# Kernel tuning notes

Measured on AMD Instinct MI355X. Metric: run time of the kernel, lower is better.

Reference implementation:

```python
import jax, jax.numpy as jnp
import numpy as np

H = 2048          # hidden_size
I = 1408          # moe_intermediate_size
E = 32            # n_routed_experts
K = 4             # num_experts_per_tok
NS = 2            # n_shared_experts
RG = RU = RD = 128  # CUR ranks
SI = I * NS       # shared-expert intermediate size
B, S = 2, 2048


def _init(key, shape, fan_in):
    return jax.random.normal(key, shape, jnp.float32) / np.sqrt(fan_in)


def setup_inputs() -> dict:
    ks = jax.random.split(jax.random.key(0), 20)
    return {
        'x': jax.random.normal(ks[0], (B, S, H), jnp.float32),
        'gate_w': _init(ks[1], (E, H), H),
        'Rg': _init(ks[2], (RG, H), H),
        'Ru': _init(ks[3], (RU, H), H),
        'Rd': _init(ks[4], (RD, I), I),
        'Ug': _init(ks[5], (E, RG, RG), RG),
        'Cg': _init(ks[6], (E, I, RG), RG),
        'Uu': _init(ks[7], (E, RU, RU), RU),
        'Cu': _init(ks[8], (E, I, RU), RU),
        'Ud': _init(ks[9], (E, RD, RD), RD),
        'Cd': _init(ks[10], (E, H, RD), RD),
        's_Rg': _init(ks[11], (RG, H), H),
        's_Ug': _init(ks[12], (RG, RG), RG),
        's_Cg': _init(ks[13], (SI, RG), RG),
        's_Ru': _init(ks[14], (RU, H), H),
        's_Uu': _init(ks[15], (RU, RU), RU),
        's_Cu': _init(ks[16], (SI, RU), RU),
        's_Rd': _init(ks[17], (RD, SI), SI),
        's_Ud': _init(ks[18], (RD, RD), RD),
        's_Cd': _init(ks[19], (H, RD), RD),
    }


def _moe_forward(x, gate_w, Rg, Ru, Rd, Ug, Cg, Uu, Cu, Ud, Cd,
                 s_Rg, s_Ug, s_Cg, s_Ru, s_Uu, s_Cu, s_Rd, s_Ud, s_Cd):
    Bv, Sv, Hv = x.shape
    xf = x.reshape(-1, Hv)                       # [T,H]
    T = xf.shape[0]

    # ---- top-k softmax gate ----
    logits = xf @ gate_w.T                       # [T,E]
    scores = jax.nn.softmax(logits, axis=-1)
    tw, ti = jax.lax.top_k(scores, K)            # [T,K]
    tw = tw / (tw.sum(-1, keepdims=True) + 1e-20)
    # dense per-(token,expert) combine weight; zero where token not routed.
    # Mathematically identical to the torch gather/per-expert-GEMM/scatter_add path.
    we = jnp.zeros((T, E), xf.dtype).at[jnp.arange(T)[:, None], ti].add(tw)  # [T,E]

    # shared R projections are expert-independent: compute once for all tokens
    rg = xf @ Rg.T                               # [T,RG]
    ru = xf @ Ru.T                               # [T,RU]

    def expert_fn(Ug_e, Cg_e, Uu_e, Cu_e, Ud_e, Cd_e, w_e, rg, ru):
        g = jax.nn.silu((rg @ Ug_e.T) @ Cg_e.T)  # [T,I]
        u = (ru @ Uu_e.T) @ Cu_e.T               # [T,I]
        rd = (g * u) @ Rd.T                      # [T,RD]
        return w_e[:, None] * ((rd @ Ud_e.T) @ Cd_e.T)  # [T,H]

    expert_fn = jax.checkpoint(expert_fn)

    def body(acc, ws):
        Ug_e, Cg_e, Uu_e, Cu_e, Ud_e, Cd_e, w_e = ws
        return acc + expert_fn(Ug_e, Cg_e, Uu_e, Cu_e, Ud_e, Cd_e, w_e, rg, ru), None

    y, _ = jax.lax.scan(body, jnp.zeros_like(xf), (Ug, Cg, Uu, Cu, Ud, Cd, we.T))

    # ---- shared experts (own R matrices, intermediate = I * n_shared) ----
    g = jax.nn.silu(((xf @ s_Rg.T) @ s_Ug.T) @ s_Cg.T)   # [T,SI]
    u = ((xf @ s_Ru.T) @ s_Uu.T) @ s_Cu.T                # [T,SI]
    sh = (((g * u) @ s_Rd.T) @ s_Ud.T) @ s_Cd.T          # [T,H]

    return (y + sh).reshape(Bv, Sv, Hv)


def reference(x, gate_w, Rg, Ru, Rd, Ug, Cg, Uu, Cu, Ud, Cd,
              s_Rg, s_Ug, s_Cg, s_Ru, s_Uu, s_Cu, s_Rd, s_Ud, s_Cd):
    return _moe_forward(x, gate_w, Rg, Ru, Rd, Ug, Cg, Uu, Cu, Ud, Cd,
                        s_Rg, s_Ug, s_Cg, s_Ru, s_Uu, s_Cu, s_Rd, s_Ud, s_Cd)
```

## Files before the change

kernel.cpp:

```cpp
#include <hip/hip_runtime.h>
#include <math.h>

#define T_TOK 4096
#define HD    2048
#define NEXP  32
#define IR    1408
#define ISH   2816
#define NPAIR (T_TOK*4)
#define SRK   136
#define MTILES 11

typedef unsigned short ushort_t;
typedef __attribute__((ext_vector_type(8))) short    short8;
typedef __attribute__((ext_vector_type(8))) __bf16   bf16x8;
typedef __attribute__((ext_vector_type(4))) float    f32x4;

__device__ __forceinline__ f32x4 MF(short8 a, short8 b, f32x4 c) {
  return __builtin_amdgcn_mfma_f32_16x16x32_bf16(
      __builtin_bit_cast(bf16x8, a), __builtin_bit_cast(bf16x8, b), c, 0, 0, 0);
}
__device__ __forceinline__ ushort_t f2b(float f) {
  unsigned u = __float_as_uint(f);
  unsigned r = (u + 0x7fffu + ((u >> 16) & 1u)) >> 16;
  return (ushort_t)r;
}
__device__ __forceinline__ float b2f(ushort_t b) {
  return __uint_as_float(((unsigned)b) << 16);
}

__device__ __forceinline__ void gll16(const ushort_t* g, ushort_t* l) {
  __builtin_amdgcn_global_load_lds(
      (const __attribute__((address_space(1))) unsigned int*)(const void*)g,
      (__attribute__((address_space(3))) unsigned int*)(void*)l, 16, 0, 0);
}

__device__ __forceinline__ void load_64x128_swz(
    const ushort_t* __restrict__ g, size_t gstride, ushort_t* lds, int tid)
{
  const int lane = tid & 63, w = tid >> 6;
  #pragma unroll
  for (int s = 0; s < 4; ++s) {
    int rbase = s*16 + w*4;
    int r = rbase + (lane >> 4);
    int p = lane & 15;
    gll16(g + (size_t)r*gstride + ((p ^ (r & 15)) << 3), lds + rbase*128);
  }
}

__device__ __forceinline__ void load_128x64_swz(
    const ushort_t* __restrict__ g, size_t gstride, ushort_t* lds, int tid)
{
  const int lane = tid & 63, w = tid >> 6;
  #pragma unroll
  for (int s = 0; s < 4; ++s) {
    int rbase = s*32 + w*8;
    int r = rbase + (lane >> 3);
    int p = lane & 7;
    gll16(g + (size_t)r*gstride + ((p ^ (r & 7)) << 3), lds + rbase*64);
  }
}

#define NSEG 19
struct CvtSegs {
  const float* s[NSEG];
  ushort_t* d[NSEG];
  int n4[NSEG];
  int blk0[NSEG+1];
};
__global__ __launch_bounds__(256) void cvt_all_kernel(CvtSegs cs)
{
  int b = blockIdx.x;
  int k = 0;
  #pragma unroll 1
  while (k+1 < NSEG && b >= cs.blk0[k+1]) ++k;
  int i = (b - cs.blk0[k])*256 + threadIdx.x;
  if (i < cs.n4[k]) {
    float4 v = ((const float4*)cs.s[k])[i];
    ushort4 o; o.x=f2b(v.x); o.y=f2b(v.y); o.z=f2b(v.z); o.w=f2b(v.w);
    ((ushort4*)cs.d[k])[i] = o;
  }
}

__global__ __launch_bounds__(256) void gate_kernel(
    const float* __restrict__ x, const float* __restrict__ gw,
    int* __restrict__ topk_idx, float* __restrict__ topk_w, int* __restrict__ cnt)
{
  __shared__ float gws[32*132];
  __shared__ float xs[4*132];
  const int tid = threadIdx.x;
  const int w = tid >> 6, lane = tid & 63;
  const int t0 = blockIdx.x * 4;
  const int e = lane & 31, half = lane >> 5;

  float acc = 0.f;
  for (int ck = 0; ck < HD/128; ++ck) {
    for (int li = tid; li < 1024; li += 256) {
      int r = li >> 5, c4 = li & 31;
      *(float4*)(gws + r*132 + c4*4) = *(const float4*)(gw + (size_t)r*HD + ck*128 + c4*4);
    }
    for (int li = tid; li < 128; li += 256) {
      int r = li >> 5, c4 = li & 31;
      *(float4*)(xs + r*132 + c4*4) = *(const float4*)(x + (size_t)(t0+r)*HD + ck*128 + c4*4);
    }
    __syncthreads();
    #pragma unroll
    for (int k4 = 0; k4 < 16; ++k4) {
      float4 xv = *(const float4*)(xs + w*132 + half*64 + k4*4);
      float4 wv = *(const float4*)(gws + e*132 + half*64 + k4*4);
      acc += xv.x*wv.x + xv.y*wv.y + xv.z*wv.z + xv.w*wv.w;
    }
    __syncthreads();
  }
  float p = acc;
  p += __shfl_down(p, 32);
  float logit = (lane < 32) ? p : -INFINITY;
  float m = logit;
  #pragma unroll
  for (int o = 32; o >= 1; o >>= 1) m = fmaxf(m, __shfl_xor(m, o));
  float ex = (lane < 32) ? expf(logit - m) : 0.f;
  float se = ex;
  #pragma unroll
  for (int o = 32; o >= 1; o >>= 1) se += __shfl_xor(se, o);
  float score = ex / se;

  bool taken = false;
  float selw[4]; int seli[4];
  for (int k = 0; k < 4; ++k) {
    float cur = (lane < 32 && !taken) ? score : -1.f;
    float mm = cur;
    #pragma unroll
    for (int o = 32; o >= 1; o >>= 1) mm = fmaxf(mm, __shfl_xor(mm, o));
    unsigned long long b = __ballot(cur == mm);
    int il = __ffsll(b) - 1;
    if (lane == il) taken = true;
    selw[k] = mm; seli[k] = il;
  }
  float wsum = selw[0]+selw[1]+selw[2]+selw[3] + 1e-20f;
  int t = t0 + w;
  if (lane < 4) {
    topk_idx[t*4+lane] = seli[lane];
    topk_w[t*4+lane]  = selw[lane] / wsum;
    atomicAdd(&cnt[seli[lane]], 1);
  }
}

__global__ void scan_kernel(const int* __restrict__ cnt, int* __restrict__ offA)
{
  if (threadIdx.x == 0) {
    int a = 0;
    for (int e = 0; e < NEXP; ++e) { offA[e] = a; a += cnt[e]; }
    offA[NEXP] = a;
  }
}

__global__ __launch_bounds__(256) void scatter_kernel(
    const int* __restrict__ topk_idx, const float* __restrict__ topk_w,
    const int* __restrict__ offA, int* __restrict__ fill,
    int* __restrict__ list_tok, int* __restrict__ slot_of)
{
  int t = blockIdx.x*256 + threadIdx.x;
  if (t >= T_TOK) return;
  #pragma unroll
  for (int k = 0; k < 4; ++k) {
    int e = topk_idx[t*4+k];
    int pos = atomicAdd(&fill[e], 1);
    int s = offA[e] + pos;
    list_tok[s] = t;
    slot_of[t*4+k] = s;
  }
}

__global__ __launch_bounds__(256) void rproj_kernel(
    const ushort_t* __restrict__ xb,
    const ushort_t* __restrict__ Rg, const ushort_t* __restrict__ Ru,
    const ushort_t* __restrict__ sRg, const ushort_t* __restrict__ sRu,
    ushort_t* __restrict__ rg, ushort_t* __restrict__ ru,
    ushort_t* __restrict__ sa, ushort_t* __restrict__ su)
{
  __shared__ ushort_t abuf[2][64*128];
  const ushort_t* W; ushort_t* Y;
  switch (blockIdx.y) {
    case 0:  W = Rg;  Y = rg; break;
    case 1:  W = Ru;  Y = ru; break;
    case 2:  W = sRg; Y = sa; break;
    default: W = sRu; Y = su; break;
  }
  const int tid = threadIdx.x;
  const int lane = tid & 63, ln = lane & 15, q = lane >> 4;
  const int wv = tid >> 6, mh = wv >> 1, nh = wv & 1;
  const int r0 = blockIdx.x * 64;

  f32x4 acc[2][4];
  #pragma unroll
  for (int i = 0; i < 2; ++i)
    #pragma unroll
    for (int j = 0; j < 4; ++j) acc[i][j] = (f32x4){0.f,0.f,0.f,0.f};

  load_64x128_swz(xb + (size_t)r0*HD, HD, abuf[0], tid);
  for (int kt = 0; kt < 16; ++kt) {
    __syncthreads();
    if (kt+1 < 16)
      load_64x128_swz(xb + (size_t)r0*HD + (kt+1)*128, HD, abuf[(kt+1)&1], tid);
    const ushort_t* A = abuf[kt&1];
    #pragma unroll
    for (int c = 0; c < 4; ++c) {
      short8 a[2], b[4];
      #pragma unroll
      for (int i = 0; i < 2; ++i) {
        int rr = mh*32 + i*16 + ln;
        a[i] = *(const short8*)(A + rr*128 + (((c*4+q) ^ (rr&15)) << 3));
      }
      #pragma unroll
      for (int j = 0; j < 4; ++j)
        b[j] = *(const short8*)(W + (size_t)(nh*64 + j*16 + ln)*HD + kt*128 + c*32 + q*8);
      #pragma unroll
      for (int i = 0; i < 2; ++i)
        #pragma unroll
        for (int j = 0; j < 4; ++j) acc[i][j] = MF(a[i], b[j], acc[i][j]);
    }
  }
  #pragma unroll
  for (int i = 0; i < 2; ++i)
    #pragma unroll
    for (int j = 0; j < 4; ++j)
      #pragma unroll
      for (int r = 0; r < 4; ++r)
        Y[(size_t)(r0 + mh*32 + i*16 + q*4 + r)*128 + nh*64 + j*16 + ln] = f2b(acc[i][j][r]);
}

__device__ __forceinline__ void gemm64x128_regs(
    int tid, const ushort_t* __restrict__ A, const ushort_t* __restrict__ Wg,
    ushort_t* __restrict__ stage, f32x4 acc[2][2][2])
{
  const int lane = tid & 63, ln = lane & 15, q = lane >> 4;
  const int wv = tid >> 6, mh = wv >> 1, nh = wv & 1;
  #pragma unroll
  for (int h = 0; h < 2; ++h)
    #pragma unroll
    for (int i = 0; i < 2; ++i)
      #pragma unroll
      for (int j = 0; j < 2; ++j) acc[h][i][j] = (f32x4){0.f,0.f,0.f,0.f};
  for (int h = 0; h < 2; ++h) {
    for (int li = tid; li < 64*16; li += 256) {
      int r = li >> 4, c = (li & 15) << 3;
      *(short8*)(stage + r*SRK + c) = *(const short8*)(Wg + (size_t)(h*64 + r)*128 + c);
    }
    __syncthreads();
    #pragma unroll
    for (int c = 0; c < 4; ++c) {
      short8 a[2], b[2];
      #pragma unroll
      for (int i = 0; i < 2; ++i)
        a[i] = *(const short8*)(A + (mh*32 + i*16 + ln)*SRK + c*32 + q*8);
      #pragma unroll
      for (int j = 0; j < 2; ++j)
        b[j] = *(const short8*)(stage + (nh*32 + j*16 + ln)*SRK + c*32 + q*8);
      #pragma unroll
      for (int i = 0; i < 2; ++i)
        #pragma unroll
        for (int j = 0; j < 2; ++j) acc[h][i][j] = MF(a[i], b[j], acc[h][i][j]);
    }
    __syncthreads();
  }
}

__global__ __launch_bounds__(256) void pair_proj_kernel(
    const ushort_t* __restrict__ rgb, const ushort_t* __restrict__ rub,
    const ushort_t* __restrict__ sab, const ushort_t* __restrict__ sub,
    const ushort_t* __restrict__ Ug, const ushort_t* __restrict__ Uu,
    const ushort_t* __restrict__ sUg, const ushort_t* __restrict__ sUu,
    const int* __restrict__ offA, const int* __restrict__ cntA,
    const int* __restrict__ list_tok,
    ushort_t* __restrict__ t1R, ushort_t* __restrict__ t2R,
    ushort_t* __restrict__ t1S, ushort_t* __restrict__ t2S)
{
  __shared__ ushort_t ldsX[64*SRK];
  __shared__ ushort_t stage[64*SRK];
  __shared__ int toks[64];
  const int tid = threadIdx.x;
  const int by = blockIdx.y;
  const bool shm = (by == NEXP);
  const int nrows = shm ? T_TOK : cntA[by];
  const int s0 = blockIdx.x * 64;
  if (s0 >= nrows) return;
  const int base = shm ? 0 : offA[by];
  const ushort_t* pUg = shm ? sUg : Ug + (size_t)by*128*128;
  const ushort_t* pUu = shm ? sUu : Uu + (size_t)by*128*128;
  const int lane = tid & 63, ln = lane & 15, q = lane >> 4;
  const int wv = tid >> 6, mh = wv >> 1, nh = wv & 1;

  if (tid < 64) {
    int sc = s0 + tid; if (sc > nrows-1) sc = nrows-1;
    toks[tid] = shm ? sc : list_tok[base + sc];
  }
  __syncthreads();

  f32x4 acc[2][2][2];
  for (int li = tid; li < 64*16; li += 256) {
    int r = li >> 4, c = (li & 15) << 3;
    const ushort_t* src = shm ? sab : rgb;
    *(short8*)(ldsX + r*SRK + c) = *(const short8*)(src + (size_t)toks[r]*128 + c);
  }
  __syncthreads();
  gemm64x128_regs(tid, ldsX, pUg, stage, acc);
  {
    ushort_t* dst = shm ? t1S : (t1R + (size_t)base*128);
    #pragma unroll
    for (int h = 0; h < 2; ++h)
      #pragma unroll
      for (int i = 0; i < 2; ++i)
        #pragma unroll
        for (int r = 0; r < 4; ++r) {
          int gs = s0 + mh*32 + i*16 + q*4 + r;
          if (gs < nrows) {
            #pragma unroll
            for (int j = 0; j < 2; ++j)
              dst[(size_t)gs*128 + h*64 + nh*32 + j*16 + ln] = f2b(acc[h][i][j][r]);
          }
        }
  }
  for (int li = tid; li < 64*16; li += 256) {
    int r = li >> 4, c = (li & 15) << 3;
    const ushort_t* src = shm ? sub : rub;
    *(short8*)(ldsX + r*SRK + c) = *(const short8*)(src + (size_t)toks[r]*128 + c);
  }
  __syncthreads();
  gemm64x128_regs(tid, ldsX, pUu, stage, acc);
  {
    ushort_t* dst = shm ? t2S : (t2R + (size_t)base*128);
    #pragma unroll
    for (int h = 0; h < 2; ++h)
      #pragma unroll
      for (int i = 0; i < 2; ++i)
        #pragma unroll
        for (int r = 0; r < 4; ++r) {
          int gs = s0 + mh*32 + i*16 + q*4 + r;
          if (gs < nrows) {
            #pragma unroll
            for (int j = 0; j < 2; ++j)
              dst[(size_t)gs*128 + h*64 + nh*32 + j*16 + ln] = f2b(acc[h][i][j][r]);
          }
        }
  }
}

__global__ __launch_bounds__(256, 2) void mid_kernel(
    const ushort_t* __restrict__ t1R, const ushort_t* __restrict__ t2R,
    const ushort_t* __restrict__ t1S, const ushort_t* __restrict__ t2S,
    const ushort_t* __restrict__ Cg, const ushort_t* __restrict__ Cu,
    const ushort_t* __restrict__ Rd,
    const ushort_t* __restrict__ sCg, const ushort_t* __restrict__ sCu,
    const ushort_t* __restrict__ sRd,
    const int* __restrict__ offA, const int* __restrict__ cntA,
    float* __restrict__ rdRp, float* __restrict__ rdSp)
{
  __shared__ ushort_t ldsCg[64*128];
  __shared__ ushort_t ldsCu[64*128];
  __shared__ ushort_t ldsRd[128*64];
  __shared__ ushort_t ldsH [64*64];

  const int tid = threadIdx.x;
  const int by = blockIdx.y, bz = blockIdx.z;
  const bool shm = (by == NEXP);
  if (bz >= (shm ? 4 : 2)) return;
  const int nrows = shm ? T_TOK : cntA[by];
  const int s0 = blockIdx.x * 64;
  if (s0 >= nrows) return;
  const int base = shm ? 0 : offA[by];
  const int Ifull = shm ? ISH : IR;
  const ushort_t* pCg = shm ? sCg : Cg + (size_t)by*IR*128;
  const ushort_t* pCu = shm ? sCu : Cu + (size_t)by*IR*128;
  const ushort_t* pRd = shm ? sRd : Rd;

  const int lane = tid & 63, ln = lane & 15, q = lane >> 4;
  const int wv = tid >> 6, mh = wv >> 1, nh = wv & 1;
  const int it0 = bz * MTILES;

  short8 t1f[2][4], t2f[2][4];
  const ushort_t* srcT1 = shm ? t1S : (t1R + (size_t)base*128);
  const ushort_t* srcT2 = shm ? t2S : (t2R + (size_t)base*128);
  #pragma unroll
  for (int i = 0; i < 2; ++i) {
    int r = s0 + mh*32 + i*16 + ln; if (r > nrows-1) r = nrows-1;
    #pragma unroll
    for (int c = 0; c < 4; ++c) {
      t1f[i][c] = *(const short8*)(srcT1 + (size_t)r*128 + c*32 + q*8);
      t2f[i][c] = *(const short8*)(srcT2 + (size_t)r*128 + c*32 + q*8);
    }
  }

  load_64x128_swz(pCg + (size_t)it0*64*128, 128, ldsCg, tid);
  load_64x128_swz(pCu + (size_t)it0*64*128, 128, ldsCu, tid);

  f32x4 rdacc[2][4];
  #pragma unroll
  for (int i = 0; i < 2; ++i)
    #pragma unroll
    for (int j = 0; j < 4; ++j) rdacc[i][j] = (f32x4){0.f,0.f,0.f,0.f};

  __syncthreads();

  for (int it = 0; it < MTILES; ++it) {
    const int i0 = (it0 + it) * 64;
    load_128x64_swz(pRd + i0, Ifull, ldsRd, tid);
    f32x4 g[2][2], u[2][2];
    #pragma unroll
    for (int i = 0; i < 2; ++i)
      #pragma unroll
      for (int j = 0; j < 2; ++j) { g[i][j] = (f32x4){0.f,0.f,0.f,0.f}; u[i][j] = (f32x4){0.f,0.f,0.f,0.f}; }
    #pragma unroll
    for (int c = 0; c < 4; ++c) {
      #pragma unroll
      for (int j = 0; j < 2; ++j) {
        int rr = nh*32 + j*16 + ln;
        int off = rr*128 + (((c*4+q) ^ (rr&15)) << 3);
        short8 bg = *(const short8*)(ldsCg + off);
        short8 bu = *(const short8*)(ldsCu + off);
        #pragma unroll
        for (int i = 0; i < 2; ++i) {
          g[i][j] = MF(t1f[i][c], bg, g[i][j]);
          u[i][j] = MF(t2f[i][c], bu, u[i][j]);
        }
      }
    }
    #pragma unroll
    for (int i = 0; i < 2; ++i)
      #pragma unroll
      for (int j = 0; j < 2; ++j)
        #pragma unroll
        for (int r = 0; r < 4; ++r) {
          float gv = g[i][j][r];
          gv = gv / (1.f + __expf(-gv));
          float hv = gv * u[i][j][r];
          int hr = mh*32 + i*16 + q*4 + r;
          int hc = nh*32 + j*16 + ln;
          ldsH[hr*64 + (((hc>>3) ^ (hr&7)) << 3) + (hc&7)] = f2b(hv);
        }
    __syncthreads();
    if (it+1 < MTILES) {
      load_64x128_swz(pCg + (size_t)(i0+64)*128, 128, ldsCg, tid);
      load_64x128_swz(pCu + (size_t)(i0+64)*128, 128, ldsCu, tid);
    }
    #pragma unroll
    for (int c2 = 0; c2 < 2; ++c2) {
      short8 a[2];
      #pragma unroll
      for (int i = 0; i < 2; ++i) {
        int rr = mh*32 + i*16 + ln;
        a[i] = *(const short8*)(ldsH + rr*64 + (((c2*4+q) ^ (rr&7)) << 3));
      }
      #pragma unroll
      for (int j = 0; j < 4; ++j) {
        int rr = nh*64 + j*16 + ln;
        short8 b = *(const short8*)(ldsRd + rr*64 + (((c2*4+q) ^ (rr&7)) << 3));
        #pragma unroll
        for (int i = 0; i < 2; ++i) rdacc[i][j] = MF(a[i], b, rdacc[i][j]);
      }
    }
    __syncthreads();
  }

  float* dst = shm ? (rdSp + (size_t)bz*T_TOK*128)
                   : (rdRp + (size_t)bz*NPAIR*128 + (size_t)base*128);
  #pragma unroll
  for (int i = 0; i < 2; ++i) {
    #pragma unroll
    for (int r = 0; r < 4; ++r) {
      int gs = s0 + mh*32 + i*16 + q*4 + r;
      if (gs < nrows) {
        #pragma unroll
        for (int j = 0; j < 4; ++j)
          dst[(size_t)gs*128 + nh*64 + j*16 + ln] = rdacc[i][j][r];
      }
    }
  }
}

__global__ __launch_bounds__(256) void out_kernel(
    const float* __restrict__ rdRp, const float* __restrict__ rdSp,
    const ushort_t* __restrict__ Ud, const ushort_t* __restrict__ Cd,
    const ushort_t* __restrict__ sUd, const ushort_t* __restrict__ sCd,
    const int* __restrict__ offA, const int* __restrict__ cntA,
    ushort_t* __restrict__ ybufR, float* __restrict__ out)
{
  __shared__ ushort_t smem[3*64*SRK];
  ushort_t* ldsA  = smem;
  ushort_t* stage = smem + 64*SRK;
  ushort_t* ldsT  = smem + 2*64*SRK;
  ushort_t* cd0   = smem;
  ushort_t* cd1   = smem + 64*128;

  const int tid = threadIdx.x;
  const int by = blockIdx.y;
  const bool shm = (by == NEXP);
  const int nrows = shm ? T_TOK : cntA[by];
  const int s0 = blockIdx.x * 64;
  if (s0 >= nrows) return;
  const int base = shm ? 0 : offA[by];
  const int ct0 = blockIdx.z * 16;
  const ushort_t* pUd = shm ? sUd : Ud + (size_t)by*128*128;
  const ushort_t* pCd = shm ? sCd : Cd + (size_t)by*HD*128;

  const int lane = tid & 63, ln = lane & 15, q = lane >> 4;
  const int wv = tid >> 6, mh = wv >> 1, nh = wv & 1;

  for (int li = tid; li < 64*32; li += 256) {
    int r = li >> 5, c4 = li & 31;
    int row = s0 + r; if (row > nrows-1) row = nrows-1;
    float4 v;
    if (shm) {
      const float* p = rdSp + (size_t)row*128 + c4*4;
      v = *(const float4*)p;
      #pragma unroll
      for (int pp = 1; pp < 4; ++pp) {
        float4 w2 = *(const float4*)(p + (size_t)pp*T_TOK*128);
        v.x += w2.x; v.y += w2.y; v.z += w2.z; v.w += w2.w;
      }
    } else {
      const float* p = rdRp + (size_t)(base+row)*128 + c4*4;
      v = *(const float4*)p;
      float4 w2 = *(const float4*)(p + (size_t)NPAIR*128);
      v.x += w2.x; v.y += w2.y; v.z += w2.z; v.w += w2.w;
    }
    ushort4 o; o.x=f2b(v.x); o.y=f2b(v.y); o.z=f2b(v.z); o.w=f2b(v.w);
    *(ushort4*)(ldsA + r*SRK + c4*4) = o;
  }
  __syncthreads();

  f32x4 acc[2][2][2];
  gemm64x128_regs(tid, ldsA, pUd, stage, acc);
  #pragma unroll
  for (int h = 0; h < 2; ++h)
    #pragma unroll
    for (int i = 0; i < 2; ++i)
      #pragma unroll
      for (int j = 0; j < 2; ++j)
        #pragma unroll
        for (int r = 0; r < 4; ++r)
          ldsT[(mh*32 + i*16 + q*4 + r)*SRK + h*64 + nh*32 + j*16 + ln] = f2b(acc[h][i][j][r]);
  __syncthreads();
  short8 t3f[2][4];
  #pragma unroll
  for (int i = 0; i < 2; ++i)
    #pragma unroll
    for (int c = 0; c < 4; ++c)
      t3f[i][c] = *(const short8*)(ldsT + (mh*32 + i*16 + ln)*SRK + c*32 + q*8);
  __syncthreads();

  load_64x128_swz(pCd + (size_t)ct0*64*128, 128, cd0, tid);
  for (int tt = 0; tt < 16; ++tt) {
    __syncthreads();
    ushort_t* cur = (tt & 1) ? cd1 : cd0;
    ushort_t* nxt = (tt & 1) ? cd0 : cd1;
    if (tt+1 < 16)
      load_64x128_swz(pCd + (size_t)(ct0+tt+1)*64*128, 128, nxt, tid);
    f32x4 y[2][2];
    #pragma unroll
    for (int i = 0; i < 2; ++i)
      #pragma unroll
      for (int j = 0; j < 2; ++j) y[i][j] = (f32x4){0.f,0.f,0.f,0.f};
    #pragma unroll
    for (int c = 0; c < 4; ++c) {
      #pragma unroll
      for (int j = 0; j < 2; ++j) {
        int rr = nh*32 + j*16 + ln;
        short8 b = *(const short8*)(cur + rr*128 + (((c*4+q) ^ (rr&15)) << 3));
        #pragma unroll
        for (int i = 0; i < 2; ++i) y[i][j] = MF(t3f[i][c], b, y[i][j]);
      }
    }
    #pragma unroll
    for (int i = 0; i < 2; ++i) {
      #pragma unroll
      for (int r = 0; r < 4; ++r) {
        int lr = mh*32 + i*16 + q*4 + r;
        int gs = s0 + lr;
        if (gs < nrows) {
          if (shm) {
            size_t ob = (size_t)gs*HD + (ct0 + tt)*64;
            #pragma unroll
            for (int j = 0; j < 2; ++j)
              out[ob + nh*32 + j*16 + ln] = y[i][j][r];
          } else {
            size_t ob = (size_t)(base + gs)*HD + (ct0 + tt)*64;
            #pragma unroll
            for (int j = 0; j < 2; ++j)
              ybufR[ob + nh*32 + j*16 + ln] = f2b(y[i][j][r]);
          }
        }
      }
    }
  }
}

__global__ __launch_bounds__(256) void combine_kernel(
    const ushort_t* __restrict__ ybufR,
    const int* __restrict__ slot_of, const float* __restrict__ topk_w,
    float* __restrict__ out)
{
  __shared__ int   ss[4];
  __shared__ float ww[4];
  const int t = blockIdx.x;
  if (threadIdx.x < 4) {
    ss[threadIdx.x] = slot_of[t*4 + threadIdx.x];
    ww[threadIdx.x] = topk_w[t*4 + threadIdx.x];
  }
  __syncthreads();
  const int c = threadIdx.x * 8;
  const size_t tb = (size_t)t*HD + c;
  float o[8];
  float4 a0 = *(const float4*)(out + tb);
  float4 a1 = *(const float4*)(out + tb + 4);
  o[0]=a0.x; o[1]=a0.y; o[2]=a0.z; o[3]=a0.w;
  o[4]=a1.x; o[5]=a1.y; o[6]=a1.z; o[7]=a1.w;
  #pragma unroll
  for (int k = 0; k < 4; ++k) {
    short8 rv = *(const short8*)(ybufR + (size_t)ss[k]*HD + c);
    float wk = ww[k];
    #pragma unroll
    for (int u = 0; u < 8; ++u)
      o[u] += wk * b2f((ushort_t)rv[u]);
  }
  float4 b0 = {o[0],o[1],o[2],o[3]};
  float4 b1 = {o[4],o[5],o[6],o[7]};
  *(float4*)(out + tb)     = b0;
  *(float4*)(out + tb + 4) = b1;
}

extern "C" void kernel_launch(void* const* d_in, const int* in_sizes, int n_in,
                              void* d_out, int out_size, void* d_ws, size_t ws_size,
                              hipStream_t stream) {
  const float* x    = (const float*)d_in[0];
  const float* gw   = (const float*)d_in[1];
  const float* Rg   = (const float*)d_in[2];
  const float* Ru   = (const float*)d_in[3];
  const float* Rd   = (const float*)d_in[4];
  const float* Ug   = (const float*)d_in[5];
  const float* Cg   = (const float*)d_in[6];
  const float* Uu   = (const float*)d_in[7];
  const float* Cu   = (const float*)d_in[8];
  const float* Ud   = (const float*)d_in[9];
  const float* Cd   = (const float*)d_in[10];
  const float* sRg  = (const float*)d_in[11];
  const float* sUg  = (const float*)d_in[12];
  const float* sCg  = (const float*)d_in[13];
  const float* sRu  = (const float*)d_in[14];
  const float* sUu  = (const float*)d_in[15];
  const float* sCu  = (const float*)d_in[16];
  const float* sRd  = (const float*)d_in[17];
  const float* sUd  = (const float*)d_in[18];
  const float* sCd  = (const float*)d_in[19];
  float* out = (float*)d_out;

  char* w = (char*)d_ws;
  auto alloc = [&](size_t bytes) -> void* {
    void* p = (void*)w; w += (bytes + 255) & ~(size_t)255; return p;
  };
  int*   cnt      = (int*)  alloc(NEXP*sizeof(int));
  int*   offA     = (int*)  alloc((NEXP+1)*sizeof(int));
  int*   fill     = (int*)  alloc(NEXP*sizeof(int));
  int*   topk_idx = (int*)  alloc((size_t)T_TOK*4*sizeof(int));
  float* topk_w   = (float*)alloc((size_t)T_TOK*4*sizeof(float));
  int*   list_tok = (int*)  alloc((size_t)NPAIR*sizeof(int));
  int*   slot_of  = (int*)  alloc((size_t)T_TOK*4*sizeof(int));
  ushort_t* xb   = (ushort_t*)alloc((size_t)T_TOK*HD*2);
  ushort_t* Rgb  = (ushort_t*)alloc((size_t)128*HD*2);
  ushort_t* Rub  = (ushort_t*)alloc((size_t)128*HD*2);
  ushort_t* Rdb  = (ushort_t*)alloc((size_t)128*IR*2);
  ushort_t* Ugb  = (ushort_t*)alloc((size_t)NEXP*128*128*2);
  ushort_t* Cgb  = (ushort_t*)alloc((size_t)NEXP*IR*128*2);
  ushort_t* Uub  = (ushort_t*)alloc((size_t)NEXP*128*128*2);
  ushort_t* Cub  = (ushort_t*)alloc((size_t)NEXP*IR*128*2);
  ushort_t* Udb  = (ushort_t*)alloc((size_t)NEXP*128*128*2);
  ushort_t* Cdb  = (ushort_t*)alloc((size_t)NEXP*HD*128*2);
  ushort_t* sRgb = (ushort_t*)alloc((size_t)128*HD*2);
  ushort_t* sUgb = (ushort_t*)alloc((size_t)128*128*2);
  ushort_t* sCgb = (ushort_t*)alloc((size_t)ISH*128*2);
  ushort_t* sRub = (ushort_t*)alloc((size_t)128*HD*2);
  ushort_t* sUub = (ushort_t*)alloc((size_t)128*128*2);
  ushort_t* sCub = (ushort_t*)alloc((size_t)ISH*128*2);
  ushort_t* sRdb = (ushort_t*)alloc((size_t)128*ISH*2);
  ushort_t* sUdb = (ushort_t*)alloc((size_t)128*128*2);
  ushort_t* sCdb = (ushort_t*)alloc((size_t)HD*128*2);
  ushort_t* rg   = (ushort_t*)alloc((size_t)T_TOK*128*2);
  ushort_t* ru   = (ushort_t*)alloc((size_t)T_TOK*128*2);
  ushort_t* sa   = (ushort_t*)alloc((size_t)T_TOK*128*2);
  ushort_t* su   = (ushort_t*)alloc((size_t)T_TOK*128*2);
  ushort_t* t1R  = (ushort_t*)alloc((size_t)NPAIR*128*2);
  ushort_t* t2R  = (ushort_t*)alloc((size_t)NPAIR*128*2);
  ushort_t* t1S  = (ushort_t*)alloc((size_t)T_TOK*128*2);
  ushort_t* t2S  = (ushort_t*)alloc((size_t)T_TOK*128*2);
  float*    rdSp = (float*)   alloc((size_t)4*T_TOK*128*sizeof(float));
  ushort_t* ybufR= (ushort_t*)alloc((size_t)NPAIR*HD*2);
  (void)ws_size; (void)in_sizes; (void)n_in;

  float* rdRp = (float*)xb;

  hipMemsetAsync(cnt,  0, NEXP*sizeof(int), stream);
  hipMemsetAsync(fill, 0, NEXP*sizeof(int), stream);

  CvtSegs cs;
  const float* ss[NSEG] = {x,Rg,Ru,Rd,Ug,Cg,Uu,Cu,Ud,Cd,sRg,sUg,sCg,sRu,sUu,sCu,sRd,sUd,sCd};
  ushort_t* dd[NSEG] = {xb,Rgb,Rub,Rdb,Ugb,Cgb,Uub,Cub,Udb,Cdb,sRgb,sUgb,sCgb,sRub,sUub,sCub,sRdb,sUdb,sCdb};
  size_t nn[NSEG] = {(size_t)T_TOK*HD,(size_t)128*HD,(size_t)128*HD,(size_t)128*IR,
                     (size_t)NEXP*128*128,(size_t)NEXP*IR*128,(size_t)NEXP*128*128,(size_t)NEXP*IR*128,
                     (size_t)NEXP*128*128,(size_t)NEXP*HD*128,(size_t)128*HD,(size_t)128*128,
                     (size_t)ISH*128,(size_t)128*HD,(size_t)128*128,(size_t)ISH*128,
                     (size_t)128*ISH,(size_t)128*128,(size_t)HD*128};
  int tot_blk = 0;
  for (int k = 0; k < NSEG; ++k) {
    cs.s[k] = ss[k]; cs.d[k] = dd[k];
    cs.n4[k] = (int)(nn[k] >> 2);
    cs.blk0[k] = tot_blk;
    tot_blk += (cs.n4[k] + 255) / 256;
  }
  cs.blk0[NSEG] = tot_blk;
  cvt_all_kernel<<<tot_blk, 256, 0, stream>>>(cs);

  gate_kernel<<<T_TOK/4, 256, 0, stream>>>(x, gw, topk_idx, topk_w, cnt);
  scan_kernel<<<1, 64, 0, stream>>>(cnt, offA);
  scatter_kernel<<<T_TOK/256, 256, 0, stream>>>(topk_idx, topk_w, offA, fill, list_tok, slot_of);
  rproj_kernel<<<dim3(T_TOK/64, 4), 256, 0, stream>>>(xb, Rgb, Rub, sRgb, sRub, rg, ru, sa, su);
  pair_proj_kernel<<<dim3(64, NEXP+1), 256, 0, stream>>>(
      rg, ru, sa, su, Ugb, Uub, sUgb, sUub, offA, cnt, list_tok, t1R, t2R, t1S, t2S);
  mid_kernel<<<dim3(64, NEXP+1, 4), 256, 0, stream>>>(
      t1R, t2R, t1S, t2S, Cgb, Cub, Rdb, sCgb, sCub, sRdb, offA, cnt, rdRp, rdSp);
  out_kernel<<<dim3(64, NEXP+1, 2), 256, 0, stream>>>(
      rdRp, rdSp, Udb, Cdb, sUdb, sCdb, offA, cnt, ybufR, out);
  combine_kernel<<<T_TOK, 256, 0, stream>>>(ybufR, slot_of, topk_w, out);
}
```

Baseline: 619.2 us.

## Read mid-kernel weights directly from global and remap blocks for XCD locality

The mid kernel drops its LDS staging of the Cg, Cu and Rd weight tiles. MFMA B-operands are now loaded straight from global memory, relying on cache hits, and the launch bound rises to 3 blocks per CU because LDS use shrinks. Both the mid and out kernels remap the linear block index so that consecutive logical blocks (same expert) land on the same XCD, improving L2 reuse of expert weights. The risk is uncoalesced, strided global loads (especially Rd with stride Ifull) and higher load latency without prefetch.

```diff
diff --git a/kernel.cpp b/kernel.cpp
--- a/kernel.cpp
+++ b/kernel.cpp
@@ -44,19 +44,6 @@
     int r = rbase + (lane >> 4);
     int p = lane & 15;
     gll16(g + (size_t)r*gstride + ((p ^ (r & 15)) << 3), lds + rbase*128);
-  }
-}
-
-__device__ __forceinline__ void load_128x64_swz(
-    const ushort_t* __restrict__ g, size_t gstride, ushort_t* lds, int tid)
-{
-  const int lane = tid & 63, w = tid >> 6;
-  #pragma unroll
-  for (int s = 0; s < 4; ++s) {
-    int rbase = s*32 + w*8;
-    int r = rbase + (lane >> 3);
-    int p = lane & 7;
-    gll16(g + (size_t)r*gstride + ((p ^ (r & 7)) << 3), lds + rbase*64);
   }
 }
 
@@ -344,7 +331,7 @@
   }
 }
 
-__global__ __launch_bounds__(256, 2) void mid_kernel(
+__global__ __launch_bounds__(256, 3) void mid_kernel(
     const ushort_t* __restrict__ t1R, const ushort_t* __restrict__ t2R,
     const ushort_t* __restrict__ t1S, const ushort_t* __restrict__ t2S,
     const ushort_t* __restrict__ Cg, const ushort_t* __restrict__ Cu,
@@ -354,17 +341,19 @@
     const int* __restrict__ offA, const int* __restrict__ cntA,
     float* __restrict__ rdRp, float* __restrict__ rdSp)
 {
-  __shared__ ushort_t ldsCg[64*128];
-  __shared__ ushort_t ldsCu[64*128];
-  __shared__ ushort_t ldsRd[128*64];
-  __shared__ ushort_t ldsH [64*64];
-
-  const int tid = threadIdx.x;
-  const int by = blockIdx.y, bz = blockIdx.z;
+  __shared__ ushort_t ldsH[64*64];
+
+  const int hh = blockIdx.x + 64*(blockIdx.y + 33*blockIdx.z);
+  const int L = (hh & 7) * 1056 + (hh >> 3);
+  const int bx  = L & 63;
+  const int rem = L >> 6;
+  const int by  = rem % 33;
+  const int bz  = rem / 33;
+
   const bool shm = (by == NEXP);
   if (bz >= (shm ? 4 : 2)) return;
   const int nrows = shm ? T_TOK : cntA[by];
-  const int s0 = blockIdx.x * 64;
+  const int s0 = bx * 64;
   if (s0 >= nrows) return;
   const int base = shm ? 0 : offA[by];
   const int Ifull = shm ? ISH : IR;
@@ -372,6 +361,7 @@
   const ushort_t* pCu = shm ? sCu : Cu + (size_t)by*IR*128;
   const ushort_t* pRd = shm ? sRd : Rd;
 
+  const int tid = threadIdx.x;
   const int lane = tid & 63, ln = lane & 15, q = lane >> 4;
   const int wv = tid >> 6, mh = wv >> 1, nh = wv & 1;
   const int it0 = bz * MTILES;
@@ -389,20 +379,17 @@
     }
   }
 
-  load_64x128_swz(pCg + (size_t)it0*64*128, 128, ldsCg, tid);
-  load_64x128_swz(pCu + (size_t)it0*64*128, 128, ldsCu, tid);
-
   f32x4 rdacc[2][4];
   #pragma unroll
   for (int i = 0; i < 2; ++i)
     #pragma unroll
     for (int j = 0; j < 4; ++j) rdacc[i][j] = (f32x4){0.f,0.f,0.f,0.f};
 
-  __syncthreads();
+  const size_t cgRow = (size_t)(nh*32 + ln)*128 + q*8;
+  const size_t rdRow = (size_t)(nh*64 + ln)*Ifull + q*8;
 
   for (int it = 0; it < MTILES; ++it) {
     const int i0 = (it0 + it) * 64;
-    load_128x64_swz(pRd + i0, Ifull, ldsRd, tid);
     f32x4 g[2][2], u[2][2];
     #pragma unroll
     for (int i = 0; i < 2; ++i)
@@ -412,10 +399,9 @@
     for (int c = 0; c < 4; ++c) {
       #pragma unroll
       for (int j = 0; j < 2; ++j) {
-        int rr = nh*32 + j*16 + ln;
-        int off = rr*128 + (((c*4+q) ^ (rr&15)) << 3);
-        short8 bg = *(const short8*)(ldsCg + off);
-        short8 bu = *(const short8*)(ldsCu + off);
+        const size_t off = (size_t)(i0 + j*16)*128 + cgRow + c*32;
+        short8 bg = *(const short8*)(pCg + off);
+        short8 bu = *(const short8*)(pCu + off);
         #pragma unroll
         for (int i = 0; i < 2; ++i) {
           g[i][j] = MF(t1f[i][c], bg, g[i][j]);
@@ -437,10 +423,6 @@
           ldsH[hr*64 + (((hc>>3) ^ (hr&7)) << 3) + (hc&7)] = f2b(hv);
         }
     __syncthreads();
-    if (it+1 < MTILES) {
-      load_64x128_swz(pCg + (size_t)(i0+64)*128, 128, ldsCg, tid);
-      load_64x128_swz(pCu + (size_t)(i0+64)*128, 128, ldsCu, tid);
-    }
     #pragma unroll
     for (int c2 = 0; c2 < 2; ++c2) {
       short8 a[2];
@@ -451,8 +433,7 @@
       }
       #pragma unroll
       for (int j = 0; j < 4; ++j) {
-        int rr = nh*64 + j*16 + ln;
-        short8 b = *(const short8*)(ldsRd + rr*64 + (((c2*4+q) ^ (rr&7)) << 3));
+        short8 b = *(const short8*)(pRd + rdRow + (size_t)(j*16)*Ifull + i0 + c2*32);
         #pragma unroll
         for (int i = 0; i < 2; ++i) rdacc[i][j] = MF(a[i], b, rdacc[i][j]);
       }
@@ -490,14 +471,20 @@
   ushort_t* cd0   = smem;
   ushort_t* cd1   = smem + 64*128;
 
+  const int hh = blockIdx.x + 64*(blockIdx.y + 33*blockIdx.z);
+  const int L = (hh & 7) * 528 + (hh >> 3);
+  const int bx  = L & 63;
+  const int rem = L >> 6;
+  const int by  = rem % 33;
+  const int bzz = rem / 33;
+
   const int tid = threadIdx.x;
-  const int by = blockIdx.y;
   const bool shm = (by == NEXP);
   const int nrows = shm ? T_TOK : cntA[by];
-  const int s0 = blockIdx.x * 64;
+  const int s0 = bx * 64;
   if (s0 >= nrows) return;
   const int base = shm ? 0 : offA[by];
-  const int ct0 = blockIdx.z * 16;
+  const int ct0 = bzz * 16;
   const ushort_t* pUd = shm ? sUd : Ud + (size_t)by*128*128;
   const ushort_t* pCd = shm ? sCd : Cd + (size_t)by*HD*128;
 
```

Result: slower. 713.0 us (+15.1%).
